# Kernel optimization log

Measured on AMD Instinct MI355X. Metric: run time of the kernel, lower is better.

## Reference

```python
import jax, jax.numpy as jnp
import numpy as np

D = 512
H = 8
HD = D // H
EPS = 1e-5
NEG_INF = -1e30


def _ln(x, g, b):
    mu = jnp.mean(x, axis=-1, keepdims=True)
    var = jnp.mean(jnp.square(x - mu), axis=-1, keepdims=True)
    return (x - mu) * jax.lax.rsqrt(var + EPS) * g + b


def setup_inputs() -> dict:
    key = jax.random.key(0)
    ks = jax.random.split(key, 8)
    V, M, S = 128, 128, 514  # seq includes 2 head tokens (cls+dist)
    inp = {
        "video_embeds": jax.random.normal(ks[0], (V, D), jnp.float32),
        "music_features": jax.random.normal(ks[1], (M, S, D), jnp.float32),
        "music_masks": jnp.ones((M, S - 2), jnp.int32),
    }
    wk = jax.random.split(ks[2], 5)
    for name, k in zip(["Wq", "Wk", "Wv", "Wo", "Wl"], wk):
        inp[name] = jax.random.normal(k, (D, D), jnp.float32) * 0.02
    for name in ["bq", "bk", "bv", "bo", "bl"]:
        inp[name] = jnp.zeros((D,), jnp.float32)
    for name in ["g1", "g2", "g3"]:
        inp[name] = jnp.ones((D,), jnp.float32)
    for name in ["b1", "b2", "b3"]:
        inp[name] = jnp.zeros((D,), jnp.float32)
    return inp


def reference(video_embeds, music_features, music_masks,
              Wq, bq, Wk, bk, Wv, bv, Wo, bo, Wl, bl,
              g1, b1, g2, b2, g3, b3):
    # drop cls + dist tokens
    mf = music_features[:, 2:, :]  # (M, f, D)
    ve = _ln(video_embeds, g1, b1)  # (V, D)
    mf = _ln(mf, g1, b1)
    V = ve.shape[0]
    M, f, _ = mf.shape

    q = (ve @ Wq.T + bq).reshape(V, H, HD).transpose(1, 0, 2)        # (H, V, hd)
    k = (mf @ Wk.T + bk).reshape(M, f, H, HD).transpose(0, 2, 1, 3)  # (M, H, f, hd)
    v = (mf @ Wv.T + bv).reshape(M, f, H, HD).transpose(0, 2, 1, 3)  # (M, H, f, hd)

    logits = jnp.einsum('hvd,mhfd->vmhf', q, k) / np.sqrt(HD).astype(np.float32)
    mask = music_masks[None, :, None, :]  # (1, M, 1, f)
    logits = jnp.where(mask == 0, NEG_INF, logits)
    w = jax.nn.softmax(logits, axis=-1)
    attn = jnp.einsum('vmhf,mhfd->vmhd', w, v).reshape(V, M, D)
    attn = attn @ Wo.T + bo

    attn = _ln(attn, g2, b2)
    out = attn + (attn @ Wl.T + bl)  # dropout = identity in eval
    return _ln(out, g3, b3)
```

## Files before the change

### kernel.cpp

```cpp
#include <hip/hip_runtime.h>
#include <hip/hip_bf16.h>

typedef unsigned int uint;
typedef unsigned short ushort;
typedef __bf16 bf16;
typedef bf16 bf16x8 __attribute__((ext_vector_type(8)));
typedef float f32x4 __attribute__((ext_vector_type(4)));
typedef ushort ushort4v __attribute__((ext_vector_type(4)));

__device__ __forceinline__ float bf2f(ushort u) {
  union { uint u; float f; } v; v.u = ((uint)u) << 16; return v.f;
}
__device__ __forceinline__ ushort f2bf(float f) {
  union { float f; uint u; } v; v.f = f;
  uint u = v.u;
  uint r = (u + 0x7fffu + ((u >> 16) & 1u)) >> 16;
  return (ushort)r;
}

__device__ __forceinline__ void gl2lds16(const void* g, void* l) {
  __builtin_amdgcn_global_load_lds(
      (const __attribute__((address_space(1))) void*)g,
      (__attribute__((address_space(3))) void*)l, 16, 0, 0);
}

__device__ __forceinline__ void ln_rows0(
    int nrows, int blk, int nblk, int tid,
    const float* __restrict__ srcA,
    const float* __restrict__ g, const float* __restrict__ b,
    ushort* __restrict__ dst)
{
  const int l = tid & 63;
  const int nw = nblk * 4;
  for (int row = blk * 4 + (tid >> 6); row < nrows; row += nw) {
    const float* s = srcA + (size_t)row * 512;
    float x[8];
    float4 a0 = *(const float4*)(s + l * 4);
    float4 a1 = *(const float4*)(s + 256 + l * 4);
    x[0] = a0.x; x[1] = a0.y; x[2] = a0.z; x[3] = a0.w;
    x[4] = a1.x; x[5] = a1.y; x[6] = a1.z; x[7] = a1.w;
    float sum = 0.f, sq = 0.f;
    #pragma unroll
    for (int j = 0; j < 8; ++j) { sum += x[j]; sq += x[j] * x[j]; }
    #pragma unroll
    for (int o = 1; o < 64; o <<= 1) {
      sum += __shfl_xor(sum, o);
      sq  += __shfl_xor(sq, o);
    }
    float mu = sum * (1.f / 512.f);
    float var = sq * (1.f / 512.f) - mu * mu;
    float rstd = rsqrtf(var + 1e-5f);
    float4 g0 = *(const float4*)(g + l * 4);
    float4 g1 = *(const float4*)(g + 256 + l * 4);
    float4 b0 = *(const float4*)(b + l * 4);
    float4 b1 = *(const float4*)(b + 256 + l * 4);
    float gv[8] = {g0.x,g0.y,g0.z,g0.w,g1.x,g1.y,g1.z,g1.w};
    float bv[8] = {b0.x,b0.y,b0.z,b0.w,b1.x,b1.y,b1.z,b1.w};
    ushort* d = dst + (size_t)row * 512;
    ushort4v p0, p1;
    #pragma unroll
    for (int j = 0; j < 4; ++j) {
      p0[j] = f2bf((x[j] - mu) * rstd * gv[j] + bv[j]);
      p1[j] = f2bf((x[4+j] - mu) * rstd * gv[4+j] + bv[4+j]);
    }
    *(ushort4v*)(d + l * 4) = p0;
    *(ushort4v*)(d + 256 + l * 4) = p1;
  }
}

__device__ __forceinline__ void ln_pair(
    int mode, int wid, int tid,
    const void* __restrict__ srcA, const void* __restrict__ srcB,
    const float* __restrict__ g, const float* __restrict__ b,
    void* __restrict__ dst)
{
  const int l = tid & 63;
  const int r0 = wid * 2, r1 = r0 + 1;
  float x0[8], x1[8];
  if (mode == 1) {
    int mm0 = r0 >> 9, fi0 = r0 & 511;
    int mm1 = r1 >> 9, fi1 = r1 & 511;
    const float* s0 = (const float*)srcA + ((size_t)mm0 * 514 + 2 + fi0) * 512;
    const float* s1 = (const float*)srcA + ((size_t)mm1 * 514 + 2 + fi1) * 512;
    float4 a0 = *(const float4*)(s0 + l * 4);
    float4 a1 = *(const float4*)(s0 + 256 + l * 4);
    float4 c0 = *(const float4*)(s1 + l * 4);
    float4 c1 = *(const float4*)(s1 + 256 + l * 4);
    x0[0]=a0.x; x0[1]=a0.y; x0[2]=a0.z; x0[3]=a0.w;
    x0[4]=a1.x; x0[5]=a1.y; x0[6]=a1.z; x0[7]=a1.w;
    x1[0]=c0.x; x1[1]=c0.y; x1[2]=c0.z; x1[3]=c0.w;
    x1[4]=c1.x; x1[5]=c1.y; x1[6]=c1.z; x1[7]=c1.w;
  } else if (mode == 2) {
    const ushort* s0 = (const ushort*)srcA + (size_t)r0 * 512;
    const ushort* s1 = (const ushort*)srcA + (size_t)r1 * 512;
    uint4 u0 = *(const uint4*)(s0 + l * 8);
    uint4 u1 = *(const uint4*)(s1 + l * 8);
    x0[0]=bf2f((ushort)u0.x); x0[1]=bf2f((ushort)(u0.x>>16));
    x0[2]=bf2f((ushort)u0.y); x0[3]=bf2f((ushort)(u0.y>>16));
    x0[4]=bf2f((ushort)u0.z); x0[5]=bf2f((ushort)(u0.z>>16));
    x0[6]=bf2f((ushort)u0.w); x0[7]=bf2f((ushort)(u0.w>>16));
    x1[0]=bf2f((ushort)u1.x); x1[1]=bf2f((ushort)(u1.x>>16));
    x1[2]=bf2f((ushort)u1.y); x1[3]=bf2f((ushort)(u1.y>>16));
    x1[4]=bf2f((ushort)u1.z); x1[5]=bf2f((ushort)(u1.z>>16));
    x1[6]=bf2f((ushort)u1.w); x1[7]=bf2f((ushort)(u1.w>>16));
  } else {
    const ushort* sa0 = (const ushort*)srcA + (size_t)r0 * 512;
    const ushort* sb0 = (const ushort*)srcB + (size_t)r0 * 512;
    const ushort* sa1 = (const ushort*)srcA + (size_t)r1 * 512;
    const ushort* sb1 = (const ushort*)srcB + (size_t)r1 * 512;
    uint4 ua0 = *(const uint4*)(sa0 + l * 8);
    uint4 ub0 = *(const uint4*)(sb0 + l * 8);
    uint4 ua1 = *(const uint4*)(sa1 + l * 8);
    uint4 ub1 = *(const uint4*)(sb1 + l * 8);
    x0[0]=bf2f((ushort)ua0.x)+bf2f((ushort)ub0.x);
    x0[1]=bf2f((ushort)(ua0.x>>16))+bf2f((ushort)(ub0.x>>16));
    x0[2]=bf2f((ushort)ua0.y)+bf2f((ushort)ub0.y);
    x0[3]=bf2f((ushort)(ua0.y>>16))+bf2f((ushort)(ub0.y>>16));
    x0[4]=bf2f((ushort)ua0.z)+bf2f((ushort)ub0.z);
    x0[5]=bf2f((ushort)(ua0.z>>16))+bf2f((ushort)(ub0.z>>16));
    x0[6]=bf2f((ushort)ua0.w)+bf2f((ushort)ub0.w);
    x0[7]=bf2f((ushort)(ua0.w>>16))+bf2f((ushort)(ub0.w>>16));
    x1[0]=bf2f((ushort)ua1.x)+bf2f((ushort)ub1.x);
    x1[1]=bf2f((ushort)(ua1.x>>16))+bf2f((ushort)(ub1.x>>16));
    x1[2]=bf2f((ushort)ua1.y)+bf2f((ushort)ub1.y);
    x1[3]=bf2f((ushort)(ua1.y>>16))+bf2f((ushort)(ub1.y>>16));
    x1[4]=bf2f((ushort)ua1.z)+bf2f((ushort)ub1.z);
    x1[5]=bf2f((ushort)(ua1.z>>16))+bf2f((ushort)(ub1.z>>16));
    x1[6]=bf2f((ushort)ua1.w)+bf2f((ushort)ub1.w);
    x1[7]=bf2f((ushort)(ua1.w>>16))+bf2f((ushort)(ub1.w>>16));
  }
  float s0 = 0.f, q0 = 0.f, s1 = 0.f, q1 = 0.f;
  #pragma unroll
  for (int j = 0; j < 8; ++j) {
    s0 += x0[j]; q0 += x0[j] * x0[j];
    s1 += x1[j]; q1 += x1[j] * x1[j];
  }
  #pragma unroll
  for (int o = 1; o < 64; o <<= 1) {
    s0 += __shfl_xor(s0, o); q0 += __shfl_xor(q0, o);
    s1 += __shfl_xor(s1, o); q1 += __shfl_xor(q1, o);
  }
  float mu0 = s0 * (1.f/512.f), mu1 = s1 * (1.f/512.f);
  float rstd0 = rsqrtf(q0 * (1.f/512.f) - mu0 * mu0 + 1e-5f);
  float rstd1 = rsqrtf(q1 * (1.f/512.f) - mu1 * mu1 + 1e-5f);

  float gv[8], bv[8];
  if (mode == 1) {
    float4 g0 = *(const float4*)(g + l * 4);
    float4 g1v = *(const float4*)(g + 256 + l * 4);
    float4 b0 = *(const float4*)(b + l * 4);
    float4 b1v = *(const float4*)(b + 256 + l * 4);
    gv[0]=g0.x; gv[1]=g0.y; gv[2]=g0.z; gv[3]=g0.w;
    gv[4]=g1v.x; gv[5]=g1v.y; gv[6]=g1v.z; gv[7]=g1v.w;
    bv[0]=b0.x; bv[1]=b0.y; bv[2]=b0.z; bv[3]=b0.w;
    bv[4]=b1v.x; bv[5]=b1v.y; bv[6]=b1v.z; bv[7]=b1v.w;
  } else {
    float4 g0 = *(const float4*)(g + l * 8);
    float4 g1v = *(const float4*)(g + l * 8 + 4);
    float4 b0 = *(const float4*)(b + l * 8);
    float4 b1v = *(const float4*)(b + l * 8 + 4);
    gv[0]=g0.x; gv[1]=g0.y; gv[2]=g0.z; gv[3]=g0.w;
    gv[4]=g1v.x; gv[5]=g1v.y; gv[6]=g1v.z; gv[7]=g1v.w;
    bv[0]=b0.x; bv[1]=b0.y; bv[2]=b0.z; bv[3]=b0.w;
    bv[4]=b1v.x; bv[5]=b1v.y; bv[6]=b1v.z; bv[7]=b1v.w;
  }
  if (mode == 1) {
    ushort* d0 = (ushort*)dst + (size_t)r0 * 512;
    ushort* d1 = (ushort*)dst + (size_t)r1 * 512;
    ushort4v p00, p01, p10, p11;
    #pragma unroll
    for (int j = 0; j < 4; ++j) {
      p00[j] = f2bf((x0[j]-mu0)*rstd0*gv[j]+bv[j]);
      p01[j] = f2bf((x0[4+j]-mu0)*rstd0*gv[4+j]+bv[4+j]);
      p10[j] = f2bf((x1[j]-mu1)*rstd1*gv[j]+bv[j]);
      p11[j] = f2bf((x1[4+j]-mu1)*rstd1*gv[4+j]+bv[4+j]);
    }
    *(ushort4v*)(d0 + l * 4) = p00;
    *(ushort4v*)(d0 + 256 + l * 4) = p01;
    *(ushort4v*)(d1 + l * 4) = p10;
    *(ushort4v*)(d1 + 256 + l * 4) = p11;
  } else if (mode == 2) {
    ushort* d0 = (ushort*)dst + (size_t)r0 * 512;
    ushort* d1 = (ushort*)dst + (size_t)r1 * 512;
    uint4 o0, o1;
    o0.x = (uint)f2bf((x0[0]-mu0)*rstd0*gv[0]+bv[0]) | ((uint)f2bf((x0[1]-mu0)*rstd0*gv[1]+bv[1]) << 16);
    o0.y = (uint)f2bf((x0[2]-mu0)*rstd0*gv[2]+bv[2]) | ((uint)f2bf((x0[3]-mu0)*rstd0*gv[3]+bv[3]) << 16);
    o0.z = (uint)f2bf((x0[4]-mu0)*rstd0*gv[4]+bv[4]) | ((uint)f2bf((x0[5]-mu0)*rstd0*gv[5]+bv[5]) << 16);
    o0.w = (uint)f2bf((x0[6]-mu0)*rstd0*gv[6]+bv[6]) | ((uint)f2bf((x0[7]-mu0)*rstd0*gv[7]+bv[7]) << 16);
    o1.x = (uint)f2bf((x1[0]-mu1)*rstd1*gv[0]+bv[0]) | ((uint)f2bf((x1[1]-mu1)*rstd1*gv[1]+bv[1]) << 16);
    o1.y = (uint)f2bf((x1[2]-mu1)*rstd1*gv[2]+bv[2]) | ((uint)f2bf((x1[3]-mu1)*rstd1*gv[3]+bv[3]) << 16);
    o1.z = (uint)f2bf((x1[4]-mu1)*rstd1*gv[4]+bv[4]) | ((uint)f2bf((x1[5]-mu1)*rstd1*gv[5]+bv[5]) << 16);
    o1.w = (uint)f2bf((x1[6]-mu1)*rstd1*gv[6]+bv[6]) | ((uint)f2bf((x1[7]-mu1)*rstd1*gv[7]+bv[7]) << 16);
    *(uint4*)(d0 + l * 8) = o0;
    *(uint4*)(d1 + l * 8) = o1;
  } else {
    float* d0 = (float*)dst + (size_t)r0 * 512;
    float* d1 = (float*)dst + (size_t)r1 * 512;
    float4 a0, a1, c0, c1;
    a0.x=(x0[0]-mu0)*rstd0*gv[0]+bv[0]; a0.y=(x0[1]-mu0)*rstd0*gv[1]+bv[1];
    a0.z=(x0[2]-mu0)*rstd0*gv[2]+bv[2]; a0.w=(x0[3]-mu0)*rstd0*gv[3]+bv[3];
    a1.x=(x0[4]-mu0)*rstd0*gv[4]+bv[4]; a1.y=(x0[5]-mu0)*rstd0*gv[5]+bv[5];
    a1.z=(x0[6]-mu0)*rstd0*gv[6]+bv[6]; a1.w=(x0[7]-mu0)*rstd0*gv[7]+bv[7];
    c0.x=(x1[0]-mu1)*rstd1*gv[0]+bv[0]; c0.y=(x1[1]-mu1)*rstd1*gv[1]+bv[1];
    c0.z=(x1[2]-mu1)*rstd1*gv[2]+bv[2]; c0.w=(x1[3]-mu1)*rstd1*gv[3]+bv[3];
    c1.x=(x1[4]-mu1)*rstd1*gv[4]+bv[4]; c1.y=(x1[5]-mu1)*rstd1*gv[5]+bv[5];
    c1.z=(x1[6]-mu1)*rstd1*gv[6]+bv[6]; c1.w=(x1[7]-mu1)*rstd1*gv[7]+bv[7];
    *(float4*)(d0 + l * 8) = a0;
    *(float4*)(d0 + l * 8 + 4) = a1;
    *(float4*)(d1 + l * 8) = c0;
    *(float4*)(d1 + l * 8 + 4) = c1;
  }
}

__global__ __launch_bounds__(256) void ln512p(
    int mode, const void* __restrict__ srcA, const void* __restrict__ srcB,
    const float* __restrict__ g, const float* __restrict__ b,
    void* __restrict__ dst)
{
  ln_pair(mode, blockIdx.x * 4 + (threadIdx.x >> 6), threadIdx.x, srcA, srcB, g, b, dst);
}

struct PreArgs {
  const float* s0; const float* s1; const float* s2; const float* s3; const float* s4;
  ushort* d0; ushort* d1; ushort* d2; ushort* d3; ushort* d4;
  const float* video; const float* music;
  const float* g1; const float* b1;
  ushort* veln; ushort* mfln;
};
__global__ __launch_bounds__(256) void preamble(PreArgs a) {
  int bb = blockIdx.x;
  if (bb < 640) {
    int t = bb * 256 + threadIdx.x;
    int which = t >> 15;
    int e = (t & 32767) * 8;
    const float* s = which == 0 ? a.s0 : which == 1 ? a.s1 : which == 2 ? a.s2 : which == 3 ? a.s3 : a.s4;
    ushort*      d = which == 0 ? a.d0 : which == 1 ? a.d1 : which == 2 ? a.d2 : which == 3 ? a.d3 : a.d4;
    float4 v0 = *(const float4*)(s + e);
    float4 v1 = *(const float4*)(s + e + 4);
    uint4 o;
    o.x = (uint)f2bf(v0.x) | ((uint)f2bf(v0.y) << 16);
    o.y = (uint)f2bf(v0.z) | ((uint)f2bf(v0.w) << 16);
    o.z = (uint)f2bf(v1.x) | ((uint)f2bf(v1.y) << 16);
    o.w = (uint)f2bf(v1.z) | ((uint)f2bf(v1.w) << 16);
    *(uint4*)(d + e) = o;
  } else if (bb < 672) {
    ln_rows0(128, bb - 640, 32, threadIdx.x, a.video, a.g1, a.b1, a.veln);
  } else {
    ln_pair(1, (bb - 672) * 4 + (threadIdx.x >> 6), threadIdx.x,
            a.music, nullptr, a.g1, a.b1, a.mfln);
  }
}

__global__ __launch_bounds__(256) void gemm_t3(
    const ushort* __restrict__ A, const ushort* __restrict__ W,
    const float* __restrict__ bias, ushort* __restrict__ C,
    float scale, int vt_mode)
{
  __shared__ __align__(16) ushort As[2][128 * 64];
  __shared__ __align__(16) ushort Bs[2][128 * 64];
  const int tid = threadIdx.x;
  const int w = tid >> 6, l = tid & 63;
  const int lg = l >> 4, lr = l & 15;
  const int wr = w >> 1, wc = w & 1;

  int nwg = gridDim.x * gridDim.y;
  int bid = blockIdx.y * gridDim.x + blockIdx.x;
  if ((nwg & 7) == 0) bid = (bid & 7) * (nwg >> 3) + (bid >> 3);
  const int bx = bid % gridDim.x, by = bid / gridDim.x;
  const int row0 = by * 128, col0 = bx * 128;

  f32x4 acc[4][4];
  #pragma unroll
  for (int i = 0; i < 4; i++)
    #pragma unroll
    for (int j = 0; j < 4; j++) { f32x4 z = {0.f,0.f,0.f,0.f}; acc[i][j] = z; }

  size_t asrc[4], wsrc[4]; int ldst[4];
  #pragma unroll
  for (int c2 = 0; c2 < 4; ++c2) {
    int c = c2 * 256 + tid;
    int r = c >> 3, j = c & 7;
    int koff = (j ^ (r & 7)) * 8;
    asrc[c2] = (size_t)(row0 + r) * 512 + koff;
    wsrc[c2] = (size_t)(col0 + r) * 512 + koff;
    ldst[c2] = (c2 * 256 + w * 64) * 8;
  }

  auto stage = [&](int pb, int kk) {
    #pragma unroll
    for (int c2 = 0; c2 < 4; ++c2) {
      gl2lds16(A + asrc[c2] + kk * 64, &As[pb][ldst[c2]]);
      gl2lds16(W + wsrc[c2] + kk * 64, &Bs[pb][ldst[c2]]);
    }
  };
  auto compute = [&](int pb) {
    #pragma unroll
    for (int ks = 0; ks < 2; ++ks) {
      bf16x8 af[4], bfr[4];
      #pragma unroll
      for (int mi = 0; mi < 4; ++mi) {
        int r = wr * 64 + mi * 16 + lr;
        af[mi] = *(const bf16x8*)(&As[pb][r * 64 + ((ks * 32 + lg * 8) ^ ((r & 7) * 8))]);
      }
      #pragma unroll
      for (int ni = 0; ni < 4; ++ni) {
        int r = wc * 64 + ni * 16 + lr;
        bfr[ni] = *(const bf16x8*)(&Bs[pb][r * 64 + ((ks * 32 + lg * 8) ^ ((r & 7) * 8))]);
      }
      #pragma unroll
      for (int mi = 0; mi < 4; ++mi)
        #pragma unroll
        for (int ni = 0; ni < 4; ++ni)
          acc[mi][ni] = __builtin_amdgcn_mfma_f32_16x16x32_bf16(af[mi], bfr[ni], acc[mi][ni], 0, 0, 0);
    }
  };

  stage(0, 0);
  __syncthreads();
  int cur = 0;
  #pragma unroll
  for (int kk = 0; kk < 7; ++kk) {
    stage(cur ^ 1, kk + 1);
    compute(cur);
    __syncthreads();
    cur ^= 1;
  }
  compute(cur);

  #pragma unroll
  for (int ni = 0; ni < 4; ++ni) {
    int cg = col0 + wc * 64 + ni * 16 + lr;
    float bc = bias[cg];
    #pragma unroll
    for (int mi = 0; mi < 4; ++mi) {
      int rg0 = row0 + wr * 64 + mi * 16 + lg * 4;
      if (!vt_mode) {
        #pragma unroll
        for (int e = 0; e < 4; ++e) {
          float v = (acc[mi][ni][e] + bc) * scale;
          C[(size_t)(rg0 + e) * 512 + cg] = f2bf(v);
        }
      } else {
        int m = rg0 >> 9, fi = rg0 & 511;
        ushort4v pk;
        #pragma unroll
        for (int e = 0; e < 4; ++e) pk[e] = f2bf((acc[mi][ni][e] + bc) * scale);
        *(ushort4v*)(C + (size_t)(m * 512 + cg) * 512 + fi) = pk;
      }
    }
  }
}

__global__ __launch_bounds__(512) void gemm_t3w(
    const ushort* __restrict__ A, const ushort* __restrict__ W,
    const float* __restrict__ bias, ushort* __restrict__ C,
    float scale, int vt_mode)
{
  __shared__ __align__(16) ushort As[2][256 * 64];
  __shared__ __align__(16) ushort Bs[2][128 * 64];
  const int tid = threadIdx.x;
  const int w = tid >> 6, l = tid & 63;
  const int lg = l >> 4, lr = l & 15;
  const int wr = w >> 1, wc = w & 1;

  int nwg = gridDim.x * gridDim.y;
  int bid = blockIdx.y * gridDim.x + blockIdx.x;
  if ((nwg & 7) == 0) bid = (bid & 7) * (nwg >> 3) + (bid >> 3);
  const int bx = bid % gridDim.x, by = bid / gridDim.x;
  const int row0 = by * 256, col0 = bx * 128;

  f32x4 acc[4][4];
  #pragma unroll
  for (int i = 0; i < 4; i++)
    #pragma unroll
    for (int j = 0; j < 4; j++) { f32x4 z = {0.f,0.f,0.f,0.f}; acc[i][j] = z; }

  size_t asrc[4], wsrc[2]; int aldst[4], wldst[2];
  {
    int r = tid >> 3, j = tid & 7;
    int koff = (j ^ (r & 7)) * 8;
    #pragma unroll
    for (int c2 = 0; c2 < 4; ++c2) {
      asrc[c2] = (size_t)(row0 + c2 * 64 + r) * 512 + koff;
      aldst[c2] = ((c2 * 64 + (w * 8)) * 64);
    }
    #pragma unroll
    for (int c2 = 0; c2 < 2; ++c2) {
      wsrc[c2] = (size_t)(col0 + c2 * 64 + r) * 512 + koff;
      wldst[c2] = ((c2 * 64 + (w * 8)) * 64);
    }
  }

  auto stage = [&](int pb, int kk) {
    #pragma unroll
    for (int c2 = 0; c2 < 4; ++c2)
      gl2lds16(A + asrc[c2] + kk * 64, &As[pb][aldst[c2] + 0]);
    #pragma unroll
    for (int c2 = 0; c2 < 2; ++c2)
      gl2lds16(W + wsrc[c2] + kk * 64, &Bs[pb][wldst[c2] + 0]);
  };
  auto compute = [&](int pb) {
    #pragma unroll
    for (int ks = 0; ks < 2; ++ks) {
      bf16x8 af[4], bfr[4];
      #pragma unroll
      for (int mi = 0; mi < 4; ++mi) {
        int r = wr * 64 + mi * 16 + lr;
        af[mi] = *(const bf16x8*)(&As[pb][r * 64 + ((ks * 32 + lg * 8) ^ ((r & 7) * 8))]);
      }
      #pragma unroll
      for (int ni = 0; ni < 4; ++ni) {
        int r = wc * 64 + ni * 16 + lr;
        bfr[ni] = *(const bf16x8*)(&Bs[pb][r * 64 + ((ks * 32 + lg * 8) ^ ((r & 7) * 8))]);
      }
      #pragma unroll
      for (int mi = 0; mi < 4; ++mi)
        #pragma unroll
        for (int ni = 0; ni < 4; ++ni)
          acc[mi][ni] = __builtin_amdgcn_mfma_f32_16x16x32_bf16(af[mi], bfr[ni], acc[mi][ni], 0, 0, 0);
    }
  };

  stage(0, 0);
  __syncthreads();
  int cur = 0;
  #pragma unroll
  for (int kk = 0; kk < 7; ++kk) {
    stage(cur ^ 1, kk + 1);
    compute(cur);
    __syncthreads();
    cur ^= 1;
  }
  compute(cur);

  #pragma unroll
  for (int ni = 0; ni < 4; ++ni) {
    int cg = col0 + wc * 64 + ni * 16 + lr;
    float bc = bias[cg];
    #pragma unroll
    for (int mi = 0; mi < 4; ++mi) {
      int rg0 = row0 + wr * 64 + mi * 16 + lg * 4;
      if (!vt_mode) {
        #pragma unroll
        for (int e = 0; e < 4; ++e) {
          float v = (acc[mi][ni][e] + bc) * scale;
          C[(size_t)(rg0 + e) * 512 + cg] = f2bf(v);
        }
      } else {
        int m = rg0 >> 9, fi = rg0 & 511;
        ushort4v pk;
        #pragma unroll
        for (int e = 0; e < 4; ++e) pk[e] = f2bf((acc[mi][ni][e] + bc) * scale);
        *(ushort4v*)(C + (size_t)(m * 512 + cg) * 512 + fi) = pk;
      }
    }
  }
}

__global__ __launch_bounds__(256) void attn_kernel(
    const ushort* __restrict__ q, const ushort* __restrict__ k,
    const ushort* __restrict__ vt, const int* __restrict__ masks,
    ushort* __restrict__ attn)
{
  __shared__ __align__(16) ushort Qs[128 * 64];
  __shared__ __align__(16) ushort Ks[64 * 64];
  __shared__ __align__(16) ushort Vs[64 * 64];
  __shared__ __align__(16) ushort Ps[4][32 * 64];
  __shared__ float maskf[64];
  __shared__ float stats[4][32];

  const int tid = threadIdx.x;
  const int w = tid >> 6, l = tid & 63;
  const int lg = l >> 4, lr = l & 15;
  const int m = blockIdx.x >> 3, h = blockIdx.x & 7;

  const size_t kbase = (size_t)(m * 512) * 512 + h * 64;
  const size_t vbase = (size_t)(m * 512 + h * 64) * 512;

  #pragma unroll
  for (int c2 = 0; c2 < 4; ++c2) {
    int c = c2 * 256 + tid;
    int r = c >> 3, j = c & 7;
    gl2lds16(q + (size_t)r * 512 + h * 64 + ((j * 8) ^ ((r & 7) * 8)),
             Qs + (c2 * 256 + w * 64) * 8);
  }

  f32x4 acc[2][4];
  #pragma unroll
  for (int i = 0; i < 2; i++)
    #pragma unroll
    for (int j = 0; j < 4; j++) { f32x4 z = {0.f,0.f,0.f,0.f}; acc[i][j] = z; }
  float m_run[2] = {-INFINITY, -INFINITY};
  float l_run[2] = {0.f, 0.f};
  bf16x8 qf[2][2];

  for (int it = 0; it < 8; ++it) {
    const int f0 = it * 64;
    #pragma unroll
    for (int c2 = 0; c2 < 2; ++c2) {
      int c = c2 * 256 + tid;
      int r = c >> 3, j = c & 7;
      int off = (j * 8) ^ ((r & 7) * 8);
      gl2lds16(k + kbase + (size_t)(f0 + r) * 512 + off, Ks + (c2 * 256 + w * 64) * 8);
      gl2lds16(vt + vbase + (size_t)r * 512 + f0 + off, Vs + (c2 * 256 + w * 64) * 8);
    }
    if (tid < 64) maskf[tid] = masks[m * 512 + f0 + tid] ? 0.f : -1e30f;
    __syncthreads();

    if (it == 0) {
      #pragma unroll
      for (int nv = 0; nv < 2; ++nv)
        #pragma unroll
        for (int k2 = 0; k2 < 2; ++k2) {
          int v = w * 32 + nv * 16 + lr;
          qf[nv][k2] = *(const bf16x8*)(Qs + v * 64 + ((k2 * 32 + lg * 8) ^ ((v & 7) * 8)));
        }
    }

    f32x4 s[4][2];
    #pragma unroll
    for (int mi = 0; mi < 4; mi++)
      #pragma unroll
      for (int nv = 0; nv < 2; nv++) { f32x4 z = {0.f,0.f,0.f,0.f}; s[mi][nv] = z; }
    #pragma unroll
    for (int k2 = 0; k2 < 2; ++k2) {
      bf16x8 kf[4];
      #pragma unroll
      for (int mi = 0; mi < 4; ++mi) {
        int f = mi * 16 + lr;
        kf[mi] = *(const bf16x8*)(Ks + f * 64 + ((k2 * 32 + lg * 8) ^ ((f & 7) * 8)));
      }
      __builtin_amdgcn_s_setprio(1);
      #pragma unroll
      for (int mi = 0; mi < 4; ++mi)
        #pragma unroll
        for (int nv = 0; nv < 2; ++nv)
          s[mi][nv] = __builtin_amdgcn_mfma_f32_16x16x32_bf16(kf[mi], qf[nv][k2], s[mi][nv], 0, 0, 0);
      __builtin_amdgcn_s_setprio(0);
    }

    float mk[4][4];
    #pragma unroll
    for (int mi = 0; mi < 4; mi++)
      #pragma unroll
      for (int e = 0; e < 4; e++) mk[mi][e] = maskf[mi * 16 + lg * 4 + e];

    #pragma unroll
    for (int nv = 0; nv < 2; ++nv) {
      float cmax = -INFINITY;
      #pragma unroll
      for (int mi = 0; mi < 4; mi++)
        #pragma unroll
        for (int e = 0; e < 4; e++) {
          s[mi][nv][e] += mk[mi][e];
          cmax = fmaxf(cmax, s[mi][nv][e]);
        }
      cmax = fmaxf(cmax, __shfl_xor(cmax, 16));
      cmax = fmaxf(cmax, __shfl_xor(cmax, 32));
      float mnew = fmaxf(m_run[nv], cmax);
      float sc = __expf(m_run[nv] - mnew);
      float csum = 0.f;
      int vloc = nv * 16 + lr;
      #pragma unroll
      for (int mi = 0; mi < 4; mi++) {
        ushort4v pk;
        #pragma unroll
        for (int e = 0; e < 4; e++) {
          float p = __expf(s[mi][nv][e] - mnew);
          csum += p;
          pk[e] = f2bf(p);
        }
        int f = mi * 16 + lg * 4;
        *(ushort4v*)(&Ps[w][vloc * 64 + (f ^ ((vloc & 7) * 8))]) = pk;
      }
      csum += __shfl_xor(csum, 16);
      csum += __shfl_xor(csum, 32);
      l_run[nv] = l_run[nv] * sc + csum;
      m_run[nv] = mnew;
      if (lg == 0) stats[w][vloc] = sc;
    }

    #pragma unroll
    for (int mi2 = 0; mi2 < 2; ++mi2)
      #pragma unroll
      for (int e = 0; e < 4; ++e) {
        float sc = stats[w][mi2 * 16 + lg * 4 + e];
        #pragma unroll
        for (int nd = 0; nd < 4; ++nd) acc[mi2][nd][e] *= sc;
      }

    #pragma unroll
    for (int k2 = 0; k2 < 2; ++k2) {
      bf16x8 pf[2], vf[4];
      #pragma unroll
      for (int mi2 = 0; mi2 < 2; ++mi2) {
        int vloc = mi2 * 16 + lr;
        pf[mi2] = *(const bf16x8*)(&Ps[w][vloc * 64 + ((k2 * 32 + lg * 8) ^ ((vloc & 7) * 8))]);
      }
      #pragma unroll
      for (int nd = 0; nd < 4; ++nd) {
        int d = nd * 16 + lr;
        vf[nd] = *(const bf16x8*)(Vs + d * 64 + ((k2 * 32 + lg * 8) ^ ((d & 7) * 8)));
      }
      __builtin_amdgcn_s_setprio(1);
      #pragma unroll
      for (int mi2 = 0; mi2 < 2; ++mi2)
        #pragma unroll
        for (int nd = 0; nd < 4; ++nd)
          acc[mi2][nd] = __builtin_amdgcn_mfma_f32_16x16x32_bf16(pf[mi2], vf[nd], acc[mi2][nd], 0, 0, 0);
      __builtin_amdgcn_s_setprio(0);
    }
    __syncthreads();
  }

  #pragma unroll
  for (int nv = 0; nv < 2; ++nv)
    if (lg == 0) stats[w][nv * 16 + lr] = 1.f / l_run[nv];
  #pragma unroll
  for (int mi2 = 0; mi2 < 2; ++mi2)
    #pragma unroll
    for (int e = 0; e < 4; ++e) {
      float invl = stats[w][mi2 * 16 + lg * 4 + e];
      int vg = w * 32 + mi2 * 16 + lg * 4 + e;
      #pragma unroll
      for (int nd = 0; nd < 4; ++nd) {
        int d = nd * 16 + lr;
        attn[(size_t)(vg * 128 + m) * 512 + h * 64 + d] = f2bf(acc[mi2][nd][e] * invl);
      }
    }
}

extern "C" void kernel_launch(void* const* d_in, const int* in_sizes, int n_in,
                              void* d_out, int out_size, void* d_ws, size_t ws_size,
                              hipStream_t stream) {
  const float* video = (const float*)d_in[0];
  const float* music = (const float*)d_in[1];
  const int*   masks = (const int*)d_in[2];
  const float* Wq = (const float*)d_in[3];
  const float* Wk = (const float*)d_in[4];
  const float* Wv = (const float*)d_in[5];
  const float* Wo = (const float*)d_in[6];
  const float* Wl = (const float*)d_in[7];
  const float* bq = (const float*)d_in[8];
  const float* bk = (const float*)d_in[9];
  const float* bv = (const float*)d_in[10];
  const float* bo = (const float*)d_in[11];
  const float* bl = (const float*)d_in[12];
  const float* g1 = (const float*)d_in[13];
  const float* g2 = (const float*)d_in[14];
  const float* g3 = (const float*)d_in[15];
  const float* b1 = (const float*)d_in[16];
  const float* b2 = (const float*)d_in[17];
  const float* b3 = (const float*)d_in[18];

  char* ws = (char*)d_ws;
  ushort* mfln = (ushort*)(ws);
  ushort* kbuf = (ushort*)(ws + 67108864);
  ushort* vtb  = (ushort*)(ws + 134217728);
  ushort* attn = (ushort*)(ws + 201326592);
  ushort* c1   = (ushort*)(ws + 218103808);
  ushort* xbuf = (ushort*)(ws + 234881024);
  ushort* veln = (ushort*)(ws + 251658240);
  ushort* qbuf = (ushort*)(ws + 251789312);
  ushort* wqb  = (ushort*)(ws + 251920384);
  ushort* wkb  = wqb + 262144;
  ushort* wvb  = wkb + 262144;
  ushort* wob  = wvb + 262144;
  ushort* wlb  = wob + 262144;

  PreArgs pa = {Wq, Wk, Wv, Wo, Wl, wqb, wkb, wvb, wob, wlb,
                video, music, g1, b1, veln, mfln};
  preamble<<<8864, 256, 0, stream>>>(pa);

  gemm_t3<<<dim3(4, 1), 256, 0, stream>>>(veln, wqb, bq, qbuf, 0.125f, 0);
  gemm_t3w<<<dim3(4, 256), 512, 0, stream>>>(mfln, wkb, bk, kbuf, 1.f, 0);
  gemm_t3w<<<dim3(4, 256), 512, 0, stream>>>(mfln, wvb, bv, vtb, 1.f, 1);

  attn_kernel<<<1024, 256, 0, stream>>>(qbuf, kbuf, vtb, masks, attn);

  gemm_t3w<<<dim3(4, 64), 512, 0, stream>>>(attn, wob, bo, c1, 1.f, 0);
  ln512p<<<2048, 256, 0, stream>>>(2, c1, nullptr, g2, b2, xbuf);
  gemm_t3w<<<dim3(4, 64), 512, 0, stream>>>(xbuf, wlb, bl, c1, 1.f, 0);
  ln512p<<<2048, 256, 0, stream>>>(3, xbuf, c1, g3, b3, d_out);
}
```

Baseline: 282.7 us.

## Fuse K/V/Q projections into one GEMM and double-buffer attention K/V tiles

Merges the separate Q, K and V projection launches into a single kernel. Each music-row tile of the LayerNormed activations is loaded once and multiplied against both Wk and Wv, and an extra grid row computes Q from the video embeddings. The attention kernel now double-buffers its K/V/mask tiles, so the next tile's global-to-LDS loads overlap the current tile's math, and the Q fragment loads are hoisted before the loop. The online softmax skips the running-max update and accumulator rescale when the new block max exceeds the old one by at most 8, which stays exact but adds register pressure, more LDS, and a Q block that reads past veln into the neighbouring buffer.

```diff
diff --git a/kernel.cpp b/kernel.cpp
--- a/kernel.cpp
+++ b/kernel.cpp
@@ -251,52 +251,68 @@
   }
 }
 
-__global__ __launch_bounds__(256) void gemm_t3(
-    const ushort* __restrict__ A, const ushort* __restrict__ W,
-    const float* __restrict__ bias, ushort* __restrict__ C,
-    float scale, int vt_mode)
+__global__ __launch_bounds__(512) void gemm_kvq(
+    const ushort* __restrict__ Amf, const ushort* __restrict__ Aq,
+    const ushort* __restrict__ Wk, const ushort* __restrict__ Wv,
+    const ushort* __restrict__ Wq,
+    const float* __restrict__ bk, const float* __restrict__ bv,
+    const float* __restrict__ bq,
+    ushort* __restrict__ K, ushort* __restrict__ Vt, ushort* __restrict__ Q)
 {
-  __shared__ __align__(16) ushort As[2][128 * 64];
-  __shared__ __align__(16) ushort Bs[2][128 * 64];
+  __shared__ __align__(16) ushort As[2][256 * 64];
+  __shared__ __align__(16) ushort Bks[2][128 * 64];
+  __shared__ __align__(16) ushort Bvs[2][128 * 64];
   const int tid = threadIdx.x;
   const int w = tid >> 6, l = tid & 63;
   const int lg = l >> 4, lr = l & 15;
   const int wr = w >> 1, wc = w & 1;
 
-  int nwg = gridDim.x * gridDim.y;
-  int bid = blockIdx.y * gridDim.x + blockIdx.x;
-  if ((nwg & 7) == 0) bid = (bid & 7) * (nwg >> 3) + (bid >> 3);
-  const int bx = bid % gridDim.x, by = bid / gridDim.x;
-  const int row0 = by * 128, col0 = bx * 128;
-
-  f32x4 acc[4][4];
+  const bool isq = (blockIdx.y == 256);
+  const int row0 = isq ? 0 : blockIdx.y * 256;
+  const int col0 = blockIdx.x * 128;
+  const ushort* Ap  = isq ? Aq : Amf;
+  const ushort* Wkp = isq ? Wq : Wk;
+
+  f32x4 kacc[4][4], vacc[4][4];
   #pragma unroll
   for (int i = 0; i < 4; i++)
     #pragma unroll
-    for (int j = 0; j < 4; j++) { f32x4 z = {0.f,0.f,0.f,0.f}; acc[i][j] = z; }
-
-  size_t asrc[4], wsrc[4]; int ldst[4];
-  #pragma unroll
-  for (int c2 = 0; c2 < 4; ++c2) {
-    int c = c2 * 256 + tid;
-    int r = c >> 3, j = c & 7;
+    for (int j = 0; j < 4; j++) {
+      f32x4 z = {0.f,0.f,0.f,0.f};
+      kacc[i][j] = z; vacc[i][j] = z;
+    }
+
+  size_t asrc[4], wksrc[2], wvsrc[2]; int aldst[4], wldst[2];
+  {
+    int r = tid >> 3, j = tid & 7;
     int koff = (j ^ (r & 7)) * 8;
-    asrc[c2] = (size_t)(row0 + r) * 512 + koff;
-    wsrc[c2] = (size_t)(col0 + r) * 512 + koff;
-    ldst[c2] = (c2 * 256 + w * 64) * 8;
+    #pragma unroll
+    for (int c2 = 0; c2 < 4; ++c2) {
+      asrc[c2] = (size_t)(row0 + c2 * 64 + r) * 512 + koff;
+      aldst[c2] = ((c2 * 64 + w * 8) * 64);
+    }
+    #pragma unroll
+    for (int c2 = 0; c2 < 2; ++c2) {
+      wksrc[c2] = (size_t)(col0 + c2 * 64 + r) * 512 + koff;
+      wvsrc[c2] = wksrc[c2];
+      wldst[c2] = ((c2 * 64 + w * 8) * 64);
+    }
   }
 
   auto stage = [&](int pb, int kk) {
     #pragma unroll
-    for (int c2 = 0; c2 < 4; ++c2) {
-      gl2lds16(A + asrc[c2] + kk * 64, &As[pb][ldst[c2]]);
-      gl2lds16(W + wsrc[c2] + kk * 64, &Bs[pb][ldst[c2]]);
+    for (int c2 = 0; c2 < 4; ++c2)
+      gl2lds16(Ap + asrc[c2] + kk * 64, &As[pb][aldst[c2]]);
+    #pragma unroll
+    for (int c2 = 0; c2 < 2; ++c2) {
+      gl2lds16(Wkp + wksrc[c2] + kk * 64, &Bks[pb][wldst[c2]]);
+      gl2lds16(Wv + wvsrc[c2] + kk * 64, &Bvs[pb][wldst[c2]]);
     }
   };
   auto compute = [&](int pb) {
     #pragma unroll
     for (int ks = 0; ks < 2; ++ks) {
-      bf16x8 af[4], bfr[4];
+      bf16x8 af[4], bkf[4];
       #pragma unroll
       for (int mi = 0; mi < 4; ++mi) {
         int r = wr * 64 + mi * 16 + lr;
@@ -305,13 +321,26 @@
       #pragma unroll
       for (int ni = 0; ni < 4; ++ni) {
         int r = wc * 64 + ni * 16 + lr;
-        bfr[ni] = *(const bf16x8*)(&Bs[pb][r * 64 + ((ks * 32 + lg * 8) ^ ((r & 7) * 8))]);
+        bkf[ni] = *(const bf16x8*)(&Bks[pb][r * 64 + ((ks * 32 + lg * 8) ^ ((r & 7) * 8))]);
       }
       #pragma unroll
       for (int mi = 0; mi < 4; ++mi)
         #pragma unroll
         for (int ni = 0; ni < 4; ++ni)
-          acc[mi][ni] = __builtin_amdgcn_mfma_f32_16x16x32_bf16(af[mi], bfr[ni], acc[mi][ni], 0, 0, 0);
+          kacc[mi][ni] = __builtin_amdgcn_mfma_f32_16x16x32_bf16(af[mi], bkf[ni], kacc[mi][ni], 0, 0, 0);
+      if (!isq) {
+        bf16x8 bvf[4];
+        #pragma unroll
+        for (int ni = 0; ni < 4; ++ni) {
+          int r = wc * 64 + ni * 16 + lr;
+          bvf[ni] = *(const bf16x8*)(&Bvs[pb][r * 64 + ((ks * 32 + lg * 8) ^ ((r & 7) * 8))]);
+        }
+        #pragma unroll
+        for (int mi = 0; mi < 4; ++mi)
+          #pragma unroll
+          for (int ni = 0; ni < 4; ++ni)
+            vacc[mi][ni] = __builtin_amdgcn_mfma_f32_16x16x32_bf16(af[mi], bvf[ni], vacc[mi][ni], 0, 0, 0);
+      }
     }
   };
 
@@ -330,22 +359,26 @@
   #pragma unroll
   for (int ni = 0; ni < 4; ++ni) {
     int cg = col0 + wc * 64 + ni * 16 + lr;
-    float bc = bias[cg];
+    float bkc = isq ? bq[cg] : bk[cg];
+    float bvc = isq ? 0.f : bv[cg];
     #pragma unroll
     for (int mi = 0; mi < 4; ++mi) {
       int rg0 = row0 + wr * 64 + mi * 16 + lg * 4;
-      if (!vt_mode) {
-        #pragma unroll
-        for (int e = 0; e < 4; ++e) {
-          float v = (acc[mi][ni][e] + bc) * scale;
-          C[(size_t)(rg0 + e) * 512 + cg] = f2bf(v);
+      if (isq) {
+        if (rg0 < 128) {
+          #pragma unroll
+          for (int e = 0; e < 4; ++e)
+            Q[(size_t)(rg0 + e) * 512 + cg] = f2bf((kacc[mi][ni][e] + bkc) * 0.125f);
         }
       } else {
+        #pragma unroll
+        for (int e = 0; e < 4; ++e)
+          K[(size_t)(rg0 + e) * 512 + cg] = f2bf(kacc[mi][ni][e] + bkc);
         int m = rg0 >> 9, fi = rg0 & 511;
         ushort4v pk;
         #pragma unroll
-        for (int e = 0; e < 4; ++e) pk[e] = f2bf((acc[mi][ni][e] + bc) * scale);
-        *(ushort4v*)(C + (size_t)(m * 512 + cg) * 512 + fi) = pk;
+        for (int e = 0; e < 4; ++e) pk[e] = f2bf(vacc[mi][ni][e] + bvc);
+        *(ushort4v*)(Vt + (size_t)(m * 512 + cg) * 512 + fi) = pk;
       }
     }
   }
@@ -394,10 +427,10 @@
   auto stage = [&](int pb, int kk) {
     #pragma unroll
     for (int c2 = 0; c2 < 4; ++c2)
-      gl2lds16(A + asrc[c2] + kk * 64, &As[pb][aldst[c2] + 0]);
+      gl2lds16(A + asrc[c2] + kk * 64, &As[pb][aldst[c2]]);
     #pragma unroll
     for (int c2 = 0; c2 < 2; ++c2)
-      gl2lds16(W + wsrc[c2] + kk * 64, &Bs[pb][wldst[c2] + 0]);
+      gl2lds16(W + wsrc[c2] + kk * 64, &Bs[pb][wldst[c2]]);
   };
   auto compute = [&](int pb) {
     #pragma unroll
@@ -463,10 +496,10 @@
     ushort* __restrict__ attn)
 {
   __shared__ __align__(16) ushort Qs[128 * 64];
-  __shared__ __align__(16) ushort Ks[64 * 64];
-  __shared__ __align__(16) ushort Vs[64 * 64];
+  __shared__ __align__(16) ushort Ks[2][64 * 64];
+  __shared__ __align__(16) ushort Vs[2][64 * 64];
   __shared__ __align__(16) ushort Ps[4][32 * 64];
-  __shared__ float maskf[64];
+  __shared__ float maskf[2][64];
   __shared__ float stats[4][32];
 
   const int tid = threadIdx.x;
@@ -476,6 +509,20 @@
 
   const size_t kbase = (size_t)(m * 512) * 512 + h * 64;
   const size_t vbase = (size_t)(m * 512 + h * 64) * 512;
+
+  int sr = tid >> 2;
+  auto stageKV = [&](int pb, int it) {
+    const int f0 = it * 64;
+    #pragma unroll
+    for (int c2 = 0; c2 < 2; ++c2) {
+      int c = c2 * 256 + tid;
+      int r = c >> 3, j = c & 7;
+      int off = (j * 8) ^ ((r & 7) * 8);
+      gl2lds16(k + kbase + (size_t)(f0 + r) * 512 + off, &Ks[pb][(c2 * 256 + w * 64) * 8]);
+      gl2lds16(vt + vbase + (size_t)r * 512 + f0 + off, &Vs[pb][(c2 * 256 + w * 64) * 8]);
+    }
+    if (tid < 64) maskf[pb][tid] = masks[m * 512 + f0 + tid] ? 0.f : -1e30f;
+  };
 
   #pragma unroll
   for (int c2 = 0; c2 < 4; ++c2) {
@@ -484,6 +531,8 @@
     gl2lds16(q + (size_t)r * 512 + h * 64 + ((j * 8) ^ ((r & 7) * 8)),
              Qs + (c2 * 256 + w * 64) * 8);
   }
+  stageKV(0, 0);
+  __syncthreads();
 
   f32x4 acc[2][4];
   #pragma unroll
@@ -493,29 +542,17 @@
   float m_run[2] = {-INFINITY, -INFINITY};
   float l_run[2] = {0.f, 0.f};
   bf16x8 qf[2][2];
-
+  #pragma unroll
+  for (int nv = 0; nv < 2; ++nv)
+    #pragma unroll
+    for (int k2 = 0; k2 < 2; ++k2) {
+      int v = w * 32 + nv * 16 + lr;
+      qf[nv][k2] = *(const bf16x8*)(Qs + v * 64 + ((k2 * 32 + lg * 8) ^ ((v & 7) * 8)));
+    }
+
+  int cur = 0;
   for (int it = 0; it < 8; ++it) {
-    const int f0 = it * 64;
-    #pragma unroll
-    for (int c2 = 0; c2 < 2; ++c2) {
-      int c = c2 * 256 + tid;
-      int r = c >> 3, j = c & 7;
-      int off = (j * 8) ^ ((r & 7) * 8);
-      gl2lds16(k + kbase + (size_t)(f0 + r) * 512 + off, Ks + (c2 * 256 + w * 64) * 8);
-      gl2lds16(vt + vbase + (size_t)r * 512 + f0 + off, Vs + (c2 * 256 + w * 64) * 8);
-    }
-    if (tid < 64) maskf[tid] = masks[m * 512 + f0 + tid] ? 0.f : -1e30f;
-    __syncthreads();
-
-    if (it == 0) {
-      #pragma unroll
-      for (int nv = 0; nv < 2; ++nv)
-        #pragma unroll
-        for (int k2 = 0; k2 < 2; ++k2) {
-          int v = w * 32 + nv * 16 + lr;
-          qf[nv][k2] = *(const bf16x8*)(Qs + v * 64 + ((k2 * 32 + lg * 8) ^ ((v & 7) * 8)));
-        }
-    }
+    if (it < 7) stageKV(cur ^ 1, it + 1);
 
     f32x4 s[4][2];
     #pragma unroll
@@ -528,7 +565,7 @@
       #pragma unroll
       for (int mi = 0; mi < 4; ++mi) {
         int f = mi * 16 + lr;
-        kf[mi] = *(const bf16x8*)(Ks + f * 64 + ((k2 * 32 + lg * 8) ^ ((f & 7) * 8)));
+        kf[mi] = *(const bf16x8*)(&Ks[cur][f * 64 + ((k2 * 32 + lg * 8) ^ ((f & 7) * 8))]);
       }
       __builtin_amdgcn_s_setprio(1);
       #pragma unroll
@@ -543,22 +580,23 @@
     #pragma unroll
     for (int mi = 0; mi < 4; mi++)
       #pragma unroll
-      for (int e = 0; e < 4; e++) mk[mi][e] = maskf[mi * 16 + lg * 4 + e];
+      for (int e = 0; e < 4; e++) mk[mi][e] = maskf[cur][mi * 16 + lg * 4 + e];
 
     #pragma unroll
     for (int nv = 0; nv < 2; ++nv) {
-      float cmax = -INFINITY;
+      float pmax = -INFINITY;
       #pragma unroll
       for (int mi = 0; mi < 4; mi++)
         #pragma unroll
         for (int e = 0; e < 4; e++) {
           s[mi][nv][e] += mk[mi][e];
-          cmax = fmaxf(cmax, s[mi][nv][e]);
+          pmax = fmaxf(pmax, s[mi][nv][e]);
         }
-      cmax = fmaxf(cmax, __shfl_xor(cmax, 16));
-      cmax = fmaxf(cmax, __shfl_xor(cmax, 32));
-      float mnew = fmaxf(m_run[nv], cmax);
-      float sc = __expf(m_run[nv] - mnew);
+      pmax = fmaxf(pmax, __shfl_xor(pmax, 16));
+      pmax = fmaxf(pmax, __shfl_xor(pmax, 32));
+      bool skip = __all(pmax - m_run[nv] <= 8.f);
+      float mnew = skip ? m_run[nv] : fmaxf(m_run[nv], pmax);
+      float sc = skip ? 1.f : __expf(m_run[nv] - mnew);
       float csum = 0.f;
       int vloc = nv * 16 + lr;
       #pragma unroll
@@ -578,16 +616,16 @@
       l_run[nv] = l_run[nv] * sc + csum;
       m_run[nv] = mnew;
       if (lg == 0) stats[w][vloc] = sc;
-    }
-
-    #pragma unroll
-    for (int mi2 = 0; mi2 < 2; ++mi2)
-      #pragma unroll
-      for (int e = 0; e < 4; ++e) {
-        float sc = stats[w][mi2 * 16 + lg * 4 + e];
-        #pragma unroll
-        for (int nd = 0; nd < 4; ++nd) acc[mi2][nd][e] *= sc;
-      }
+      if (!skip) {
+        int mi2 = nv;
+        #pragma unroll
+        for (int e = 0; e < 4; ++e) {
+          float scv = stats[w][mi2 * 16 + lg * 4 + e];
+          #pragma unroll
+          for (int nd = 0; nd < 4; ++nd) acc[mi2][nd][e] *= scv;
+        }
+      }
+    }
 
     #pragma unroll
     for (int k2 = 0; k2 < 2; ++k2) {
@@ -600,7 +638,7 @@
       #pragma unroll
       for (int nd = 0; nd < 4; ++nd) {
         int d = nd * 16 + lr;
-        vf[nd] = *(const bf16x8*)(Vs + d * 64 + ((k2 * 32 + lg * 8) ^ ((d & 7) * 8)));
+        vf[nd] = *(const bf16x8*)(&Vs[cur][d * 64 + ((k2 * 32 + lg * 8) ^ ((d & 7) * 8))]);
       }
       __builtin_amdgcn_s_setprio(1);
       #pragma unroll
@@ -611,6 +649,7 @@
       __builtin_amdgcn_s_setprio(0);
     }
     __syncthreads();
+    cur ^= 1;
   }
 
   #pragma unroll
@@ -672,9 +711,8 @@
                 video, music, g1, b1, veln, mfln};
   preamble<<<8864, 256, 0, stream>>>(pa);
 
-  gemm_t3<<<dim3(4, 1), 256, 0, stream>>>(veln, wqb, bq, qbuf, 0.125f, 0);
-  gemm_t3w<<<dim3(4, 256), 512, 0, stream>>>(mfln, wkb, bk, kbuf, 1.f, 0);
-  gemm_t3w<<<dim3(4, 256), 512, 0, stream>>>(mfln, wvb, bv, vtb, 1.f, 1);
+  gemm_kvq<<<dim3(4, 257), 512, 0, stream>>>(
+      mfln, veln, wkb, wvb, wqb, bk, bv, bq, kbuf, vtb, qbuf);
 
   attn_kernel<<<1024, 256, 0, stream>>>(qbuf, kbuf, vtb, masks, attn);
 
```

New measurement: 271.7 us. 3.9% less time.
